# Performance work log

Measured on AMD Instinct MI355X. Metric: run time of the kernel, lower is better.

The kernel has to match this reference:

```python
import jax, jax.numpy as jnp
import numpy as np

U, I, H, E = 50000, 50000, 128, 800000


def segment_softmax(vals, seg, num):
    m = jax.ops.segment_max(vals, seg, num_segments=num)
    ex = jnp.exp(vals - m[seg])
    s = jax.ops.segment_sum(ex, seg, num_segments=num)
    return ex / s[seg]


def setup_inputs() -> dict:
    key = jax.random.key(0)
    ks = jax.random.split(key, 16)
    scale = 1.0 / np.sqrt(H)
    inp = {
        "u_emb": jax.random.normal(ks[0], (U, H), jnp.float32),
        "i_emb": jax.random.normal(ks[1], (I, H), jnp.float32),
        "pVui": jax.random.normal(ks[2], (E, H), jnp.float32),
        "pKiu": jax.random.normal(ks[3], (E, H), jnp.float32),
        "w1": jax.random.normal(ks[4], (H, H), jnp.float32) * scale,
        "w2": jax.random.normal(ks[5], (H, H), jnp.float32) * scale,
        "w1b": jax.random.normal(ks[6], (H, H), jnp.float32) * scale,
        "w2b": jax.random.normal(ks[7], (H, H), jnp.float32) * scale,
        "w3": jax.random.normal(ks[8], (H, H), jnp.float32) * scale,
        "w4": jax.random.normal(ks[9], (H, H), jnp.float32) * scale,
        "edge_index": jax.random.randint(ks[10], (2, E), 0, min(U, I), jnp.int64),
        "last_u": jax.random.randint(ks[11], (2, U), 0, I, jnp.int64),
        "last_i": jax.random.randint(ks[12], (2, I), 0, U, jnp.int64),
        "graph": jnp.zeros((1,), jnp.int64),
    }
    return inp


def reference(u_emb, i_emb, pVui, pKiu, w1, w2, w1b, w2b, w3, w4,
              edge_index, last_u, last_i, graph):
    sqrt_d = np.sqrt(float(u_emb.shape[1])).astype if False else float(np.sqrt(u_emb.shape[1]))
    nu, ni = u_emb.shape[0], i_emb.shape[0]
    src_u, dst_i = edge_index[0], edge_index[1]  # per-edge (user, item)

    # ---- longterm ----
    um_att = u_emb @ w2.T            # [U,H]
    im_att = i_emb @ w1.T            # [I,H]
    # sparse_dense_mul(edge_index, um_att @ im_att.T) -> per-edge dot products
    e_vals = jnp.sum(um_att[src_u] * im_att[dst_i], axis=-1)  # [E]
    e_ui = e_vals + jnp.sum(um_att[src_u] * pVui, axis=-1)
    alphas = segment_softmax(e_ui / sqrt_d, src_u, nu)        # softmax over items per user
    e_iu = e_vals + jnp.sum(im_att[dst_i] * pKiu, axis=-1)
    betas = segment_softmax(e_iu / sqrt_d, dst_i, ni)         # softmax over users per item
    um_b = u_emb @ w2b.T
    im_b = i_emb @ w1b.T
    hLu = jax.ops.segment_sum(alphas[:, None] * (im_b[dst_i] + pKiu), src_u, num_segments=nu)
    hLi = jax.ops.segment_sum(betas[:, None] * (um_b[src_u] + pVui), dst_i, num_segments=ni)

    # ---- shortterm ----
    last_item = i_emb[last_u[1]] @ w3.T   # [U,H] last item embedding per user
    last_user = u_emb[last_i[1]] @ w4.T   # [I,H] last user embedding per item
    a_vals = jnp.sum(last_item[src_u] * im_att[dst_i], axis=-1)
    s_alphas = segment_softmax(a_vals / sqrt_d, src_u, nu)
    b_vals = jnp.sum(last_user[src_u] * im_att[dst_i], axis=-1)
    s_betas = segment_softmax(b_vals / sqrt_d, dst_i, ni)
    # pass_messages with p = ones -> messages + 1
    hSu = jax.ops.segment_sum(s_alphas[:, None] * (im_att[dst_i] + 1.0), src_u, num_segments=nu)
    hSi = jax.ops.segment_sum(s_betas[:, None] * (um_att[src_u] + 1.0), dst_i, num_segments=ni)
    return (hLu, hSu, hLi, hSi)
```

## Files before the change

kernel.cpp:

```cpp
#include <hip/hip_runtime.h>
#include <hip/hip_bf16.h>
#include <math.h>


#define WB 1024

typedef float fvec4 __attribute__((ext_vector_type(4)));

__device__ __forceinline__ float4 nt_load4(const float* p) {
    fvec4 v = __builtin_nontemporal_load((const fvec4*)p);
    return make_float4(v.x, v.y, v.z, v.w);
}
__device__ __forceinline__ float dot4(float4 a, float4 b) {
    return a.x * b.x + a.y * b.y + a.z * b.z + a.w * b.w;
}
__device__ __forceinline__ void bfu(uint4 v, float4& lo, float4& hi) {
    lo.x = __uint_as_float(v.x << 16);
    lo.y = __uint_as_float(v.x & 0xFFFF0000u);
    lo.z = __uint_as_float(v.y << 16);
    lo.w = __uint_as_float(v.y & 0xFFFF0000u);
    hi.x = __uint_as_float(v.z << 16);
    hi.y = __uint_as_float(v.z & 0xFFFF0000u);
    hi.z = __uint_as_float(v.w << 16);
    hi.w = __uint_as_float(v.w & 0xFFFF0000u);
}
__device__ __forceinline__ unsigned rne16(float f) {
    unsigned u = __float_as_uint(f);
    return (u + 0x7FFFu + ((u >> 16) & 1u)) >> 16;
}
__device__ __forceinline__ unsigned pack2(float a, float b) {
    return rne16(a) | (rne16(b) << 16);
}

__global__ __launch_bounds__(256) void zero_kernel(int* __restrict__ p, int n)
{
    int i = blockIdx.x * 256 + threadIdx.x;
    if (i < n) p[i] = 0;
}

struct Gemm6Desc {
    const float* X[6];
    const float* W[6];
    unsigned short* O[6];
    const int*   g[6];
    int          ostride[6];
    int          nrows[6];
};

__global__ __launch_bounds__(256) void gemm6_kernel(Gemm6Desc d)
{
    __shared__ float Xl[64 * 32];
    __shared__ float Wl[128 * 32];
    const int j6 = blockIdx.y;
    const float* __restrict__ X = d.X[j6];
    const float* __restrict__ W = d.W[j6];
    unsigned short* __restrict__ O = d.O[j6];
    const int* __restrict__ gidx = d.g[j6];
    const int ostride = d.ostride[j6];
    const int nrows   = d.nrows[j6];

    const int t  = threadIdx.x;
    const int tx = t & 15;
    const int ty = t >> 4;
    const int brow = blockIdx.x * 64;
    if (brow >= nrows) return;

    float acc[4][8];
#pragma unroll
    for (int j = 0; j < 4; ++j)
#pragma unroll
        for (int i = 0; i < 8; ++i) acc[j][i] = 0.f;

    for (int k0 = 0; k0 < 128; k0 += 32) {
        __syncthreads();
#pragma unroll
        for (int u = 0; u < 2; ++u) {
            int idx4 = t + u * 256;
            int r  = idx4 >> 3;
            int k4 = idx4 & 7;
            int row = brow + r;
            float4 v = make_float4(0.f, 0.f, 0.f, 0.f);
            if (row < nrows) {
                int g = gidx ? gidx[row] : row;
                v = *(const float4*)(X + (size_t)g * 128 + k0 + k4 * 4);
            }
            int sw = k4 ^ ((r >> 3) & 7);
            *(float4*)(Xl + r * 32 + sw * 4) = v;
        }
#pragma unroll
        for (int u = 0; u < 4; ++u) {
            int idx4 = t + u * 256;
            int c  = idx4 >> 3;
            int k4 = idx4 & 7;
            float4 v = *(const float4*)(W + (size_t)c * 128 + k0 + k4 * 4);
            int sw = k4 ^ ((c >> 3) & 7);
            *(float4*)(Wl + c * 32 + sw * 4) = v;
        }
        __syncthreads();
#pragma unroll
        for (int k4 = 0; k4 < 8; ++k4) {
            float4 xv[4], wv[8];
#pragma unroll
            for (int j = 0; j < 4; ++j) {
                int r = ty * 4 + j;
                xv[j] = *(const float4*)(Xl + r * 32 + ((k4 ^ ((r >> 3) & 7)) * 4));
            }
#pragma unroll
            for (int i = 0; i < 8; ++i) {
                int c = tx * 8 + i;
                wv[i] = *(const float4*)(Wl + c * 32 + ((k4 ^ ((c >> 3) & 7)) * 4));
            }
#pragma unroll
            for (int j = 0; j < 4; ++j)
#pragma unroll
                for (int i = 0; i < 8; ++i) {
                    acc[j][i] += xv[j].x * wv[i].x;
                    acc[j][i] += xv[j].y * wv[i].y;
                    acc[j][i] += xv[j].z * wv[i].z;
                    acc[j][i] += xv[j].w * wv[i].w;
                }
        }
    }
    const int base = (tx < 8) ? (16 * tx) : (16 * (tx - 8) + 4);
#pragma unroll
    for (int j = 0; j < 4; ++j) {
        int row = brow + ty * 4 + j;
        if (row < nrows) {
            unsigned short* op = O + (size_t)row * ostride;
            uint2 lo, hi;
            lo.x = pack2(acc[j][0], acc[j][1]);
            lo.y = pack2(acc[j][2], acc[j][3]);
            hi.x = pack2(acc[j][4], acc[j][5]);
            hi.y = pack2(acc[j][6], acc[j][7]);
            *(uint2*)(op + base)     = lo;
            *(uint2*)(op + base + 8) = hi;
        }
    }
}

__global__ __launch_bounds__(256) void hist_kernel(
    const int* __restrict__ ei, int E,
    int* __restrict__ deg_u, int* __restrict__ deg_i)
{
    int e = blockIdx.x * 256 + threadIdx.x;
    if (e < E) {
        atomicAdd(&deg_u[ei[e]], 1);
        atomicAdd(&deg_i[ei[E + e]], 1);
    }
}

__global__ __launch_bounds__(256) void scan_blocksums_kernel(
    const int* __restrict__ deg_u, int nu, int nbu,
    const int* __restrict__ deg_i, int ni,
    int* __restrict__ bsum)
{
    int b = blockIdx.x;
    const int* deg; int n; int base;
    if (b < nbu) { deg = deg_u; n = nu; base = b * WB; }
    else         { deg = deg_i; n = ni; base = (b - nbu) * WB; }
    int t = threadIdx.x;
    int s = 0;
#pragma unroll
    for (int j = 0; j < 4; ++j) {
        int i = base + t * 4 + j;
        if (i < n) s += deg[i];
    }
#pragma unroll
    for (int o = 32; o > 0; o >>= 1) s += __shfl_xor(s, o);
    __shared__ int wt[4];
    if ((t & 63) == 0) wt[t >> 6] = s;
    __syncthreads();
    if (t == 0) bsum[b] = wt[0] + wt[1] + wt[2] + wt[3];
}

__global__ void scan_partials_kernel(
    const int* __restrict__ bsum, int* __restrict__ bscan,
    int nbu, int nbi,
    int* __restrict__ off_u, int nu, int* __restrict__ off_i, int ni)
{
    if (threadIdx.x != 0) return;
    if (blockIdx.x == 0) {
        int c = 0;
        for (int b = 0; b < nbu; ++b) { bscan[b] = c; c += bsum[b]; }
        off_u[nu] = c;
    } else {
        int c = 0;
        for (int b = 0; b < nbi; ++b) { bscan[nbu + b] = c; c += bsum[nbu + b]; }
        off_i[ni] = c;
    }
}

__global__ __launch_bounds__(256) void scan_final_kernel(
    const int* __restrict__ deg_u, int nu, int nbu,
    const int* __restrict__ deg_i, int ni,
    const int* __restrict__ bscan,
    int* __restrict__ off_u, int* __restrict__ cur_u,
    int* __restrict__ off_i, int* __restrict__ cur_i)
{
    int b = blockIdx.x;
    const int* deg; int n; int base; int* off; int* cur;
    if (b < nbu) { deg = deg_u; n = nu; base = b * WB; off = off_u; cur = cur_u; }
    else         { deg = deg_i; n = ni; base = (b - nbu) * WB; off = off_i; cur = cur_i; }
    int t = threadIdx.x;
    int lane = t & 63, w = t >> 6;
    int v[4];
    int s = 0;
#pragma unroll
    for (int j = 0; j < 4; ++j) {
        int i = base + t * 4 + j;
        v[j] = (i < n) ? deg[i] : 0;
        s += v[j];
    }
    int inc = s;
#pragma unroll
    for (int o = 1; o < 64; o <<= 1) {
        int x = __shfl_up(inc, o);
        if (lane >= o) inc += x;
    }
    int excl = inc - s;
    __shared__ int wt[4];
    if (lane == 63) wt[w] = inc;
    __syncthreads();
    int wbase = 0;
    for (int j = 0; j < w; ++j) wbase += wt[j];
    int e = bscan[b] + wbase + excl;
#pragma unroll
    for (int j = 0; j < 4; ++j) {
        int i = base + t * 4 + j;
        if (i < n) { off[i] = e; cur[i] = e; }
        e += v[j];
    }
}

__global__ __launch_bounds__(256) void scatter_ids_kernel(
    const int* __restrict__ ei, int E,
    int* __restrict__ cur_u, int* __restrict__ cur_i,
    int2* __restrict__ eu_list, int2* __restrict__ ei_list)
{
    int e = blockIdx.x * 256 + threadIdx.x;
    if (e < E) {
        int u = ei[e], v = ei[E + e];
        int pu = atomicAdd(&cur_u[u], 1);
        eu_list[pu] = make_int2(v, e);
        int pi = atomicAdd(&cur_i[v], 1);
        ei_list[pi] = make_int2(u, e);
    }
}

__global__ __launch_bounds__(256) void gather_u_kernel(
    const unsigned short* __restrict__ fusedU,
    const unsigned short* __restrict__ fusedI,
    const unsigned short* __restrict__ last_item,
    const unsigned short* __restrict__ last_user,
    const float* __restrict__ pVui, const float* __restrict__ pKiu,
    const int2* __restrict__ lst, const int* __restrict__ off_u,
    float2* __restrict__ x24,
    float* __restrict__ hLu, float* __restrict__ hSu, int U, float inv_sqrt_d)
{
    const int wv   = (int)(((size_t)blockIdx.x * blockDim.x + threadIdx.x) >> 6);
    const int lane = threadIdx.x & 63;
    const int g = lane >> 4;
    const int q = lane & 15;
    const int uid = wv * 4 + g;
    if (uid >= U) return;

    const uint4 umP = ((const uint4*)(fusedU    + (size_t)uid * 256))[q];
    const uint4 liP = ((const uint4*)(last_item + (size_t)uid * 128))[q];
    const uint4 luP = ((const uint4*)(last_user + (size_t)uid * 128))[q];

    float4 a1l = make_float4(0.f,0.f,0.f,0.f), a1h = make_float4(0.f,0.f,0.f,0.f);
    float4 a3l = make_float4(0.f,0.f,0.f,0.f), a3h = make_float4(0.f,0.f,0.f,0.f);
    float s1 = 0.f, s3 = 0.f;
    const int e0 = off_u[uid], e1 = off_u[uid + 1];

    int eA = e0, eB = e0 + 1;
    bool vA = eA < e1, vB = eB < e1;
    int2 rA = vA ? lst[eA] : make_int2(0, 0);
    int2 rB = vB ? lst[eB] : rA;

    while (vA) {
        int eA2 = eA + 2, eB2 = eB + 2;
        bool vA2 = eA2 < e1, vB2 = eB2 < e1;
        int2 rA2 = vA2 ? lst[eA2] : make_int2(0, 0);
        int2 rB2 = vB2 ? lst[eB2] : rA2;

        const uint4* fIA = (const uint4*)(fusedI + (size_t)rA.x * 256);
        const float* pvA = pVui + (size_t)rA.y * 128;
        const float* pkA = pKiu + (size_t)rA.y * 128;
        const uint4* fIB = (const uint4*)(fusedI + (size_t)rB.x * 256);
        const float* pvB = pVui + (size_t)rB.y * 128;
        const float* pkB = pKiu + (size_t)rB.y * 128;

        uint4 iaAp = fIA[q], ibAp = fIA[16 + q];
        uint4 iaBp = fIB[q], ibBp = fIB[16 + q];
        float4 pvA0 = nt_load4(pvA + q * 4), pvA1 = nt_load4(pvA + 64 + q * 4);
        float4 pkA0 = nt_load4(pkA + q * 4), pkA1 = nt_load4(pkA + 64 + q * 4);
        float4 pvB0 = nt_load4(pvB + q * 4), pvB1 = nt_load4(pvB + 64 + q * 4);
        float4 pkB0 = nt_load4(pkB + q * 4), pkB1 = nt_load4(pkB + 64 + q * 4);

        float4 iaA0, iaA1, iaB0, iaB1;
        bfu(iaAp, iaA0, iaA1);
        bfu(iaBp, iaB0, iaB1);

        float4 t0, t1;
        bfu(umP, t0, t1);
        float dA0 = dot4(t0, iaA0) + dot4(t1, iaA1);
        float qA1 = dA0 + dot4(t0, pvA0) + dot4(t1, pvA1);
        float dB0 = dot4(t0, iaB0) + dot4(t1, iaB1);
        float qB1 = dB0 + dot4(t0, pvB0) + dot4(t1, pvB1);
        float qA2 = dA0 + dot4(iaA0, pkA0) + dot4(iaA1, pkA1);
        float qB2 = dB0 + dot4(iaB0, pkB0) + dot4(iaB1, pkB1);
        bfu(liP, t0, t1);
        float qA3 = dot4(t0, iaA0) + dot4(t1, iaA1);
        float qB3 = dot4(t0, iaB0) + dot4(t1, iaB1);
        bfu(luP, t0, t1);
        float qA4 = dot4(t0, iaA0) + dot4(t1, iaA1);
        float qB4 = dot4(t0, iaB0) + dot4(t1, iaB1);
#pragma unroll
        for (int o = 8; o > 0; o >>= 1) {
            qA1 += __shfl_xor(qA1, o); qA2 += __shfl_xor(qA2, o);
            qA3 += __shfl_xor(qA3, o); qA4 += __shfl_xor(qA4, o);
            qB1 += __shfl_xor(qB1, o); qB2 += __shfl_xor(qB2, o);
            qB3 += __shfl_xor(qB3, o); qB4 += __shfl_xor(qB4, o);
        }
        float x1A = __expf(qA1 * inv_sqrt_d);
        float x2A = __expf(qA2 * inv_sqrt_d);
        float x3A = __expf(qA3 * inv_sqrt_d);
        float x4A = __expf(qA4 * inv_sqrt_d);
        float mB  = vB ? 1.f : 0.f;
        float x1B = __expf(qB1 * inv_sqrt_d) * mB;
        float x2B = __expf(qB2 * inv_sqrt_d);
        float x3B = __expf(qB3 * inv_sqrt_d) * mB;
        float x4B = __expf(qB4 * inv_sqrt_d);

        float4 ibA0, ibA1, ibB0, ibB1;
        bfu(ibAp, ibA0, ibA1);
        bfu(ibBp, ibB0, ibB1);
        a1l.x += x1A*(ibA0.x+pkA0.x) + x1B*(ibB0.x+pkB0.x);
        a1l.y += x1A*(ibA0.y+pkA0.y) + x1B*(ibB0.y+pkB0.y);
        a1l.z += x1A*(ibA0.z+pkA0.z) + x1B*(ibB0.z+pkB0.z);
        a1l.w += x1A*(ibA0.w+pkA0.w) + x1B*(ibB0.w+pkB0.w);
        a1h.x += x1A*(ibA1.x+pkA1.x) + x1B*(ibB1.x+pkB1.x);
        a1h.y += x1A*(ibA1.y+pkA1.y) + x1B*(ibB1.y+pkB1.y);
        a1h.z += x1A*(ibA1.z+pkA1.z) + x1B*(ibB1.z+pkB1.z);
        a1h.w += x1A*(ibA1.w+pkA1.w) + x1B*(ibB1.w+pkB1.w);
        a3l.x += x3A*(iaA0.x+1.f) + x3B*(iaB0.x+1.f);
        a3l.y += x3A*(iaA0.y+1.f) + x3B*(iaB0.y+1.f);
        a3l.z += x3A*(iaA0.z+1.f) + x3B*(iaB0.z+1.f);
        a3l.w += x3A*(iaA0.w+1.f) + x3B*(iaB0.w+1.f);
        a3h.x += x3A*(iaA1.x+1.f) + x3B*(iaB1.x+1.f);
        a3h.y += x3A*(iaA1.y+1.f) + x3B*(iaB1.y+1.f);
        a3h.z += x3A*(iaA1.z+1.f) + x3B*(iaB1.z+1.f);
        a3h.w += x3A*(iaA1.w+1.f) + x3B*(iaB1.w+1.f);
        s1 += x1A + x1B; s3 += x3A + x3B;
        if (q == 0) {
            x24[rA.y] = make_float2(x2A, x4A);
            if (vB) x24[rB.y] = make_float2(x2B, x4B);
        }
        eA = eA2; eB = eB2; vA = vA2; vB = vB2; rA = rA2; rB = rB2;
    }
    float r1 = (s1 > 0.f) ? 1.f / s1 : 0.f;
    float r3 = (s3 > 0.f) ? 1.f / s3 : 0.f;
    float4* oL = (float4*)(hLu + (size_t)uid * 128);
    float4* oS = (float4*)(hSu + (size_t)uid * 128);
    oL[q]      = make_float4(a1l.x*r1, a1l.y*r1, a1l.z*r1, a1l.w*r1);
    oL[q + 16] = make_float4(a1h.x*r1, a1h.y*r1, a1h.z*r1, a1h.w*r1);
    oS[q]      = make_float4(a3l.x*r3, a3l.y*r3, a3l.z*r3, a3l.w*r3);
    oS[q + 16] = make_float4(a3h.x*r3, a3h.y*r3, a3h.z*r3, a3h.w*r3);
}

__global__ __launch_bounds__(256) void gather_i_kernel(
    const unsigned short* __restrict__ fusedU,
    const float* __restrict__ pVui,
    const int2* __restrict__ lst, const int* __restrict__ off_i,
    const float2* __restrict__ x24,
    float* __restrict__ hLi, float* __restrict__ hSi, int I)
{
    const int wv   = (int)(((size_t)blockIdx.x * blockDim.x + threadIdx.x) >> 6);
    const int lane = threadIdx.x & 63;
    const int g = lane >> 4;
    const int q = lane & 15;
    const int iid = wv * 4 + g;
    if (iid >= I) return;

    float4 a2l = make_float4(0.f,0.f,0.f,0.f), a2h = make_float4(0.f,0.f,0.f,0.f);
    float4 a4l = make_float4(0.f,0.f,0.f,0.f), a4h = make_float4(0.f,0.f,0.f,0.f);
    float s2 = 0.f, s4 = 0.f;
    const int e0 = off_i[iid], e1 = off_i[iid + 1];

    int eA = e0, eB = e0 + 1;
    bool vA = eA < e1, vB = eB < e1;
    int2 rA = vA ? lst[eA] : make_int2(0, 0);
    int2 rB = vB ? lst[eB] : rA;
    float2 xA = vA ? x24[rA.y] : make_float2(0.f, 0.f);
    float2 xB = vB ? x24[rB.y] : make_float2(0.f, 0.f);

    while (vA) {
        int eA2 = eA + 2, eB2 = eB + 2;
        bool vA2 = eA2 < e1, vB2 = eB2 < e1;
        int2 rA2 = vA2 ? lst[eA2] : make_int2(0, 0);
        int2 rB2 = vB2 ? lst[eB2] : rA2;
        float2 xA2v = vA2 ? x24[rA2.y] : make_float2(0.f, 0.f);
        float2 xB2v = vB2 ? x24[rB2.y] : make_float2(0.f, 0.f);

        const uint4* fUA = (const uint4*)(fusedU + (size_t)rA.x * 256);
        const float* pvA = pVui + (size_t)rA.y * 128;
        const uint4* fUB = (const uint4*)(fusedU + (size_t)rB.x * 256);
        const float* pvB = pVui + (size_t)rB.y * 128;

        uint4 uaAp = fUA[q], ubAp = fUA[16 + q];
        uint4 uaBp = fUB[q], ubBp = fUB[16 + q];
        float4 pvA0 = nt_load4(pvA + q * 4), pvA1 = nt_load4(pvA + 64 + q * 4);
        float4 pvB0 = nt_load4(pvB + q * 4), pvB1 = nt_load4(pvB + 64 + q * 4);

        float4 uaA0, uaA1, ubA0, ubA1, uaB0, uaB1, ubB0, ubB1;
        bfu(uaAp, uaA0, uaA1); bfu(ubAp, ubA0, ubA1);
        bfu(uaBp, uaB0, uaB1); bfu(ubBp, ubB0, ubB1);

        if (!vB) { xB.x = 0.f; xB.y = 0.f; }
        a2l.x += xA.x*(ubA0.x+pvA0.x) + xB.x*(ubB0.x+pvB0.x);
        a2l.y += xA.x*(ubA0.y+pvA0.y) + xB.x*(ubB0.y+pvB0.y);
        a2l.z += xA.x*(ubA0.z+pvA0.z) + xB.x*(ubB0.z+pvB0.z);
        a2l.w += xA.x*(ubA0.w+pvA0.w) + xB.x*(ubB0.w+pvB0.w);
        a2h.x += xA.x*(ubA1.x+pvA1.x) + xB.x*(ubB1.x+pvB1.x);
        a2h.y += xA.x*(ubA1.y+pvA1.y) + xB.x*(ubB1.y+pvB1.y);
        a2h.z += xA.x*(ubA1.z+pvA1.z) + xB.x*(ubB1.z+pvB1.z);
        a2h.w += xA.x*(ubA1.w+pvA1.w) + xB.x*(ubB1.w+pvB1.w);
        a4l.x += xA.y*(uaA0.x+1.f) + xB.y*(uaB0.x+1.f);
        a4l.y += xA.y*(uaA0.y+1.f) + xB.y*(uaB0.y+1.f);
        a4l.z += xA.y*(uaA0.z+1.f) + xB.y*(uaB0.z+1.f);
        a4l.w += xA.y*(uaA0.w+1.f) + xB.y*(uaB0.w+1.f);
        a4h.x += xA.y*(uaA1.x+1.f) + xB.y*(uaB1.x+1.f);
        a4h.y += xA.y*(uaA1.y+1.f) + xB.y*(uaB1.y+1.f);
        a4h.z += xA.y*(uaA1.z+1.f) + xB.y*(uaB1.z+1.f);
        a4h.w += xA.y*(uaA1.w+1.f) + xB.y*(uaB1.w+1.f);
        s2 += xA.x + xB.x; s4 += xA.y + xB.y;

        eA = eA2; eB = eB2; vA = vA2; vB = vB2;
        rA = rA2; rB = rB2; xA = xA2v; xB = xB2v;
    }
    float r2 = (s2 > 0.f) ? 1.f / s2 : 0.f;
    float r4 = (s4 > 0.f) ? 1.f / s4 : 0.f;
    float4* oL = (float4*)(hLi + (size_t)iid * 128);
    float4* oS = (float4*)(hSi + (size_t)iid * 128);
    oL[q]      = make_float4(a2l.x*r2, a2l.y*r2, a2l.z*r2, a2l.w*r2);
    oL[q + 16] = make_float4(a2h.x*r2, a2h.y*r2, a2h.z*r2, a2h.w*r2);
    oS[q]      = make_float4(a4l.x*r4, a4l.y*r4, a4l.z*r4, a4l.w*r4);
    oS[q + 16] = make_float4(a4h.x*r4, a4h.y*r4, a4h.z*r4, a4h.w*r4);
}

extern "C" void kernel_launch(void* const* d_in, const int* in_sizes, int n_in,
                              void* d_out, int out_size, void* d_ws, size_t ws_size,
                              hipStream_t stream)
{
    const float* u_emb = (const float*)d_in[0];
    const float* i_emb = (const float*)d_in[1];
    const float* pVui  = (const float*)d_in[2];
    const float* pKiu  = (const float*)d_in[3];
    const float* w1    = (const float*)d_in[4];
    const float* w2    = (const float*)d_in[5];
    const float* w1b   = (const float*)d_in[6];
    const float* w2b   = (const float*)d_in[7];
    const float* w3    = (const float*)d_in[8];
    const float* w4    = (const float*)d_in[9];
    const int* edge_index = (const int*)d_in[10];
    const int* last_u     = (const int*)d_in[11];
    const int* last_i     = (const int*)d_in[12];

    const int U = in_sizes[0] / 128;
    const int I = in_sizes[1] / 128;
    const int E = in_sizes[10] / 2;
    const int nbu = (U + WB - 1) / WB;
    const int nbi = (I + WB - 1) / WB;

    unsigned short* us = (unsigned short*)d_ws;
    unsigned short* fusedU    = us;  us += (size_t)U * 256;
    unsigned short* fusedI    = us;  us += (size_t)I * 256;
    unsigned short* last_item = us;  us += (size_t)U * 128;
    unsigned short* last_user = us;  us += (size_t)I * 128;
    float* ws = (float*)us;
    float2* x24 = (float2*)ws;  ws += (size_t)E * 2;
    int2* eu_list = (int2*)ws;  ws += (size_t)E * 2;
    int2* ei_list = (int2*)ws;  ws += (size_t)E * 2;
    int* ip = (int*)ws;
    int* deg_u   = ip;  ip += U;
    int* deg_i   = ip;  ip += I;
    int* off_u   = ip;  ip += U + 1;
    int* off_i   = ip;  ip += I + 1;
    int* cur_u   = ip;  ip += U;
    int* cur_i   = ip;  ip += I;
    int* bsum    = ip;  ip += nbu + nbi;
    int* bscan   = ip;  ip += nbu + nbi;

    float* hLu = (float*)d_out;
    float* hSu = hLu + (size_t)U * 128;
    float* hLi = hSu + (size_t)U * 128;
    float* hSi = hLi + (size_t)I * 128;

    dim3 blk(256);
    const int eblk = (E + 255) / 256;
    zero_kernel<<<(U + I + 255) / 256, blk, 0, stream>>>(deg_u, U + I);
    hist_kernel<<<eblk, blk, 0, stream>>>(edge_index, E, deg_u, deg_i);
    scan_blocksums_kernel<<<nbu + nbi, blk, 0, stream>>>(deg_u, U, nbu, deg_i, I, bsum);
    scan_partials_kernel<<<2, 64, 0, stream>>>(bsum, bscan, nbu, nbi, off_u, U, off_i, I);
    scan_final_kernel<<<nbu + nbi, blk, 0, stream>>>(
        deg_u, U, nbu, deg_i, I, bscan, off_u, cur_u, off_i, cur_i);
    scatter_ids_kernel<<<eblk, blk, 0, stream>>>(
        edge_index, E, cur_u, cur_i, eu_list, ei_list);

    Gemm6Desc gd;
    gd.X[0] = u_emb; gd.W[0] = w2;  gd.O[0] = fusedU;       gd.g[0] = nullptr;    gd.ostride[0] = 256; gd.nrows[0] = U;
    gd.X[1] = u_emb; gd.W[1] = w2b; gd.O[1] = fusedU + 128; gd.g[1] = nullptr;    gd.ostride[1] = 256; gd.nrows[1] = U;
    gd.X[2] = i_emb; gd.W[2] = w1;  gd.O[2] = fusedI;       gd.g[2] = nullptr;    gd.ostride[2] = 256; gd.nrows[2] = I;
    gd.X[3] = i_emb; gd.W[3] = w1b; gd.O[3] = fusedI + 128; gd.g[3] = nullptr;    gd.ostride[3] = 256; gd.nrows[3] = I;
    gd.X[4] = i_emb; gd.W[4] = w3;  gd.O[4] = last_item;    gd.g[4] = last_u + U; gd.ostride[4] = 128; gd.nrows[4] = U;
    gd.X[5] = u_emb; gd.W[5] = w4;  gd.O[5] = last_user;    gd.g[5] = last_i + I; gd.ostride[5] = 128; gd.nrows[5] = I;
    int maxrows = (U > I) ? U : I;
    dim3 ggrid((maxrows + 63) / 64, 6);
    gemm6_kernel<<<ggrid, blk, 0, stream>>>(gd);

    const float inv_sqrt_d = 1.0f / sqrtf(128.0f);
    gather_u_kernel<<<(U + 15) / 16, blk, 0, stream>>>(
        fusedU, fusedI, last_item, last_user, pVui, pKiu, eu_list, off_u,
        x24, hLu, hSu, U, inv_sqrt_d);
    gather_i_kernel<<<(I + 15) / 16, blk, 0, stream>>>(
        fusedU, pVui, ei_list, off_i, x24, hLi, hSi, I);
}
```

Baseline: 709.3 us.

## Merge user and item gathers into one kernel, recomputing item scores

The separate user-side and item-side gather kernels are replaced by a single kernel whose blocks alternate between user segments and item segments, so both sides run concurrently in one launch. The x24 per-edge buffer of item softmax numerators is removed. The item side now recomputes its scores itself, gathering pKiu and last_user rows per edge. This drops the x24 write/read and the ordering dependency between the two kernels. In exchange, the item pass must stream all of pKiu a second time, adding a large amount of memory traffic.

New measurement: 871.2 us. 1.23x slower.

```diff
diff --git a/kernel.cpp b/kernel.cpp
--- a/kernel.cpp
+++ b/kernel.cpp
@@ -247,206 +247,213 @@
     }
 }
 
-__global__ __launch_bounds__(256) void gather_u_kernel(
+__global__ __launch_bounds__(256) void mega_gather_kernel(
     const unsigned short* __restrict__ fusedU,
     const unsigned short* __restrict__ fusedI,
     const unsigned short* __restrict__ last_item,
     const unsigned short* __restrict__ last_user,
     const float* __restrict__ pVui, const float* __restrict__ pKiu,
-    const int2* __restrict__ lst, const int* __restrict__ off_u,
-    float2* __restrict__ x24,
-    float* __restrict__ hLu, float* __restrict__ hSu, int U, float inv_sqrt_d)
-{
-    const int wv   = (int)(((size_t)blockIdx.x * blockDim.x + threadIdx.x) >> 6);
+    const int2* __restrict__ eu_list, const int* __restrict__ off_u,
+    const int2* __restrict__ ei_list, const int* __restrict__ off_i,
+    float* __restrict__ hLu, float* __restrict__ hSu,
+    float* __restrict__ hLi, float* __restrict__ hSi,
+    int U, int I, int nu_blk, int ni_blk, float inv_sqrt_d)
+{
+    const int bid = blockIdx.x;
+    int sel, blk;
+    const int mn = (nu_blk < ni_blk) ? nu_blk : ni_blk;
+    if (bid < 2 * mn) { sel = bid & 1; blk = bid >> 1; }
+    else {
+        int r = bid - 2 * mn;
+        if (nu_blk > ni_blk) { sel = 0; blk = mn + r; }
+        else                 { sel = 1; blk = mn + r; }
+    }
     const int lane = threadIdx.x & 63;
     const int g = lane >> 4;
     const int q = lane & 15;
-    const int uid = wv * 4 + g;
-    if (uid >= U) return;
-
-    const uint4 umP = ((const uint4*)(fusedU    + (size_t)uid * 256))[q];
-    const uint4 liP = ((const uint4*)(last_item + (size_t)uid * 128))[q];
-    const uint4 luP = ((const uint4*)(last_user + (size_t)uid * 128))[q];
-
-    float4 a1l = make_float4(0.f,0.f,0.f,0.f), a1h = make_float4(0.f,0.f,0.f,0.f);
-    float4 a3l = make_float4(0.f,0.f,0.f,0.f), a3h = make_float4(0.f,0.f,0.f,0.f);
-    float s1 = 0.f, s3 = 0.f;
-    const int e0 = off_u[uid], e1 = off_u[uid + 1];
-
-    int eA = e0, eB = e0 + 1;
-    bool vA = eA < e1, vB = eB < e1;
-    int2 rA = vA ? lst[eA] : make_int2(0, 0);
-    int2 rB = vB ? lst[eB] : rA;
-
-    while (vA) {
-        int eA2 = eA + 2, eB2 = eB + 2;
-        bool vA2 = eA2 < e1, vB2 = eB2 < e1;
-        int2 rA2 = vA2 ? lst[eA2] : make_int2(0, 0);
-        int2 rB2 = vB2 ? lst[eB2] : rA2;
-
-        const uint4* fIA = (const uint4*)(fusedI + (size_t)rA.x * 256);
-        const float* pvA = pVui + (size_t)rA.y * 128;
-        const float* pkA = pKiu + (size_t)rA.y * 128;
-        const uint4* fIB = (const uint4*)(fusedI + (size_t)rB.x * 256);
-        const float* pvB = pVui + (size_t)rB.y * 128;
-        const float* pkB = pKiu + (size_t)rB.y * 128;
-
-        uint4 iaAp = fIA[q], ibAp = fIA[16 + q];
-        uint4 iaBp = fIB[q], ibBp = fIB[16 + q];
-        float4 pvA0 = nt_load4(pvA + q * 4), pvA1 = nt_load4(pvA + 64 + q * 4);
-        float4 pkA0 = nt_load4(pkA + q * 4), pkA1 = nt_load4(pkA + 64 + q * 4);
-        float4 pvB0 = nt_load4(pvB + q * 4), pvB1 = nt_load4(pvB + 64 + q * 4);
-        float4 pkB0 = nt_load4(pkB + q * 4), pkB1 = nt_load4(pkB + 64 + q * 4);
-
-        float4 iaA0, iaA1, iaB0, iaB1;
-        bfu(iaAp, iaA0, iaA1);
-        bfu(iaBp, iaB0, iaB1);
-
-        float4 t0, t1;
-        bfu(umP, t0, t1);
-        float dA0 = dot4(t0, iaA0) + dot4(t1, iaA1);
-        float qA1 = dA0 + dot4(t0, pvA0) + dot4(t1, pvA1);
-        float dB0 = dot4(t0, iaB0) + dot4(t1, iaB1);
-        float qB1 = dB0 + dot4(t0, pvB0) + dot4(t1, pvB1);
-        float qA2 = dA0 + dot4(iaA0, pkA0) + dot4(iaA1, pkA1);
-        float qB2 = dB0 + dot4(iaB0, pkB0) + dot4(iaB1, pkB1);
-        bfu(liP, t0, t1);
-        float qA3 = dot4(t0, iaA0) + dot4(t1, iaA1);
-        float qB3 = dot4(t0, iaB0) + dot4(t1, iaB1);
-        bfu(luP, t0, t1);
-        float qA4 = dot4(t0, iaA0) + dot4(t1, iaA1);
-        float qB4 = dot4(t0, iaB0) + dot4(t1, iaB1);
-#pragma unroll
-        for (int o = 8; o > 0; o >>= 1) {
-            qA1 += __shfl_xor(qA1, o); qA2 += __shfl_xor(qA2, o);
-            qA3 += __shfl_xor(qA3, o); qA4 += __shfl_xor(qA4, o);
-            qB1 += __shfl_xor(qB1, o); qB2 += __shfl_xor(qB2, o);
-            qB3 += __shfl_xor(qB3, o); qB4 += __shfl_xor(qB4, o);
+    const int seg = blk * 16 + (threadIdx.x >> 6) * 4 + g;
+
+    if (sel == 0) {
+        const int uid = seg;
+        if (uid >= U) return;
+        const uint4 umP = ((const uint4*)(fusedU    + (size_t)uid * 256))[q];
+        const uint4 liP = ((const uint4*)(last_item + (size_t)uid * 128))[q];
+
+        float4 a1l = make_float4(0.f,0.f,0.f,0.f), a1h = make_float4(0.f,0.f,0.f,0.f);
+        float4 a3l = make_float4(0.f,0.f,0.f,0.f), a3h = make_float4(0.f,0.f,0.f,0.f);
+        float s1 = 0.f, s3 = 0.f;
+        const int e0 = off_u[uid], e1 = off_u[uid + 1];
+
+        int eA = e0, eB = e0 + 1;
+        bool vA = eA < e1, vB = eB < e1;
+        int2 rA = vA ? eu_list[eA] : make_int2(0, 0);
+        int2 rB = vB ? eu_list[eB] : rA;
+
+        while (vA) {
+            int eA2 = eA + 2, eB2 = eB + 2;
+            bool vA2 = eA2 < e1, vB2 = eB2 < e1;
+            int2 rA2 = vA2 ? eu_list[eA2] : make_int2(0, 0);
+            int2 rB2 = vB2 ? eu_list[eB2] : rA2;
+
+            const uint4* fIA = (const uint4*)(fusedI + (size_t)rA.x * 256);
+            const float* pvA = pVui + (size_t)rA.y * 128;
+            const float* pkA = pKiu + (size_t)rA.y * 128;
+            const uint4* fIB = (const uint4*)(fusedI + (size_t)rB.x * 256);
+            const float* pvB = pVui + (size_t)rB.y * 128;
+            const float* pkB = pKiu + (size_t)rB.y * 128;
+
+            uint4 iaAp = fIA[q], ibAp = fIA[16 + q];
+            uint4 iaBp = fIB[q], ibBp = fIB[16 + q];
+            float4 pvA0 = nt_load4(pvA + q * 4), pvA1 = nt_load4(pvA + 64 + q * 4);
+            float4 pkA0 = nt_load4(pkA + q * 4), pkA1 = nt_load4(pkA + 64 + q * 4);
+            float4 pvB0 = nt_load4(pvB + q * 4), pvB1 = nt_load4(pvB + 64 + q * 4);
+            float4 pkB0 = nt_load4(pkB + q * 4), pkB1 = nt_load4(pkB + 64 + q * 4);
+
+            float4 iaA0, iaA1, iaB0, iaB1, t0, t1;
+            bfu(iaAp, iaA0, iaA1);
+            bfu(iaBp, iaB0, iaB1);
+            bfu(umP, t0, t1);
+            float qA1 = dot4(t0, iaA0) + dot4(t1, iaA1)
+                      + dot4(t0, pvA0) + dot4(t1, pvA1);
+            float qB1 = dot4(t0, iaB0) + dot4(t1, iaB1)
+                      + dot4(t0, pvB0) + dot4(t1, pvB1);
+            bfu(liP, t0, t1);
+            float qA3 = dot4(t0, iaA0) + dot4(t1, iaA1);
+            float qB3 = dot4(t0, iaB0) + dot4(t1, iaB1);
+#pragma unroll
+            for (int o = 8; o > 0; o >>= 1) {
+                qA1 += __shfl_xor(qA1, o); qA3 += __shfl_xor(qA3, o);
+                qB1 += __shfl_xor(qB1, o); qB3 += __shfl_xor(qB3, o);
+            }
+            float x1A = __expf(qA1 * inv_sqrt_d);
+            float x3A = __expf(qA3 * inv_sqrt_d);
+            float mB  = vB ? 1.f : 0.f;
+            float x1B = __expf(qB1 * inv_sqrt_d) * mB;
+            float x3B = __expf(qB3 * inv_sqrt_d) * mB;
+
+            float4 ibA0, ibA1, ibB0, ibB1;
+            bfu(ibAp, ibA0, ibA1);
+            bfu(ibBp, ibB0, ibB1);
+            a1l.x += x1A*(ibA0.x+pkA0.x) + x1B*(ibB0.x+pkB0.x);
+            a1l.y += x1A*(ibA0.y+pkA0.y) + x1B*(ibB0.y+pkB0.y);
+            a1l.z += x1A*(ibA0.z+pkA0.z) + x1B*(ibB0.z+pkB0.z);
+            a1l.w += x1A*(ibA0.w+pkA0.w) + x1B*(ibB0.w+pkB0.w);
+            a1h.x += x1A*(ibA1.x+pkA1.x) + x1B*(ibB1.x+pkB1.x);
+            a1h.y += x1A*(ibA1.y+pkA1.y) + x1B*(ibB1.y+pkB1.y);
+            a1h.z += x1A*(ibA1.z+pkA1.z) + x1B*(ibB1.z+pkB1.z);
+            a1h.w += x1A*(ibA1.w+pkA1.w) + x1B*(ibB1.w+pkB1.w);
+            a3l.x += x3A*(iaA0.x+1.f) + x3B*(iaB0.x+1.f);
+            a3l.y += x3A*(iaA0.y+1.f) + x3B*(iaB0.y+1.f);
+            a3l.z += x3A*(iaA0.z+1.f) + x3B*(iaB0.z+1.f);
+            a3l.w += x3A*(iaA0.w+1.f) + x3B*(iaB0.w+1.f);
+            a3h.x += x3A*(iaA1.x+1.f) + x3B*(iaB1.x+1.f);
+            a3h.y += x3A*(iaA1.y+1.f) + x3B*(iaB1.y+1.f);
+            a3h.z += x3A*(iaA1.z+1.f) + x3B*(iaB1.z+1.f);
+            a3h.w += x3A*(iaA1.w+1.f) + x3B*(iaB1.w+1.f);
+            s1 += x1A + x1B; s3 += x3A + x3B;
+
+            eA = eA2; eB = eB2; vA = vA2; vB = vB2; rA = rA2; rB = rB2;
         }
-        float x1A = __expf(qA1 * inv_sqrt_d);
-        float x2A = __expf(qA2 * inv_sqrt_d);
-        float x3A = __expf(qA3 * inv_sqrt_d);
-        float x4A = __expf(qA4 * inv_sqrt_d);
-        float mB  = vB ? 1.f : 0.f;
-        float x1B = __expf(qB1 * inv_sqrt_d) * mB;
-        float x2B = __expf(qB2 * inv_sqrt_d);
-        float x3B = __expf(qB3 * inv_sqrt_d) * mB;
-        float x4B = __expf(qB4 * inv_sqrt_d);
-
-        float4 ibA0, ibA1, ibB0, ibB1;
-        bfu(ibAp, ibA0, ibA1);
-        bfu(ibBp, ibB0, ibB1);
-        a1l.x += x1A*(ibA0.x+pkA0.x) + x1B*(ibB0.x+pkB0.x);
-        a1l.y += x1A*(ibA0.y+pkA0.y) + x1B*(ibB0.y+pkB0.y);
-        a1l.z += x1A*(ibA0.z+pkA0.z) + x1B*(ibB0.z+pkB0.z);
-        a1l.w += x1A*(ibA0.w+pkA0.w) + x1B*(ibB0.w+pkB0.w);
-        a1h.x += x1A*(ibA1.x+pkA1.x) + x1B*(ibB1.x+pkB1.x);
-        a1h.y += x1A*(ibA1.y+pkA1.y) + x1B*(ibB1.y+pkB1.y);
-        a1h.z += x1A*(ibA1.z+pkA1.z) + x1B*(ibB1.z+pkB1.z);
-        a1h.w += x1A*(ibA1.w+pkA1.w) + x1B*(ibB1.w+pkB1.w);
-        a3l.x += x3A*(iaA0.x+1.f) + x3B*(iaB0.x+1.f);
-        a3l.y += x3A*(iaA0.y+1.f) + x3B*(iaB0.y+1.f);
-        a3l.z += x3A*(iaA0.z+1.f) + x3B*(iaB0.z+1.f);
-        a3l.w += x3A*(iaA0.w+1.f) + x3B*(iaB0.w+1.f);
-        a3h.x += x3A*(iaA1.x+1.f) + x3B*(iaB1.x+1.f);
-        a3h.y += x3A*(iaA1.y+1.f) + x3B*(iaB1.y+1.f);
-        a3h.z += x3A*(iaA1.z+1.f) + x3B*(iaB1.z+1.f);
-        a3h.w += x3A*(iaA1.w+1.f) + x3B*(iaB1.w+1.f);
-        s1 += x1A + x1B; s3 += x3A + x3B;
-        if (q == 0) {
-            x24[rA.y] = make_float2(x2A, x4A);
-            if (vB) x24[rB.y] = make_float2(x2B, x4B);
+        float r1 = (s1 > 0.f) ? 1.f / s1 : 0.f;
+        float r3 = (s3 > 0.f) ? 1.f / s3 : 0.f;
+        float4* oL = (float4*)(hLu + (size_t)uid * 128);
+        float4* oS = (float4*)(hSu + (size_t)uid * 128);
+        oL[q]      = make_float4(a1l.x*r1, a1l.y*r1, a1l.z*r1, a1l.w*r1);
+        oL[q + 16] = make_float4(a1h.x*r1, a1h.y*r1, a1h.z*r1, a1h.w*r1);
+        oS[q]      = make_float4(a3l.x*r3, a3l.y*r3, a3l.z*r3, a3l.w*r3);
+        oS[q + 16] = make_float4(a3h.x*r3, a3h.y*r3, a3h.z*r3, a3h.w*r3);
+    } else {
+        const int iid = seg;
+        if (iid >= I) return;
+        const uint4 imP = ((const uint4*)(fusedI + (size_t)iid * 256))[q];
+
+        float4 a2l = make_float4(0.f,0.f,0.f,0.f), a2h = make_float4(0.f,0.f,0.f,0.f);
+        float4 a4l = make_float4(0.f,0.f,0.f,0.f), a4h = make_float4(0.f,0.f,0.f,0.f);
+        float s2 = 0.f, s4 = 0.f;
+        const int e0 = off_i[iid], e1 = off_i[iid + 1];
+
+        int eA = e0, eB = e0 + 1;
+        bool vA = eA < e1, vB = eB < e1;
+        int2 rA = vA ? ei_list[eA] : make_int2(0, 0);
+        int2 rB = vB ? ei_list[eB] : rA;
+
+        while (vA) {
+            int eA2 = eA + 2, eB2 = eB + 2;
+            bool vA2 = eA2 < e1, vB2 = eB2 < e1;
+            int2 rA2 = vA2 ? ei_list[eA2] : make_int2(0, 0);
+            int2 rB2 = vB2 ? ei_list[eB2] : rA2;
+
+            const uint4* fUA = (const uint4*)(fusedU + (size_t)rA.x * 256);
+            const float* pvA = pVui + (size_t)rA.y * 128;
+            const float* pkA = pKiu + (size_t)rA.y * 128;
+            const uint4 luAp = ((const uint4*)(last_user + (size_t)rA.x * 128))[q];
+            const uint4* fUB = (const uint4*)(fusedU + (size_t)rB.x * 256);
+            const float* pvB = pVui + (size_t)rB.y * 128;
+            const float* pkB = pKiu + (size_t)rB.y * 128;
+            const uint4 luBp = ((const uint4*)(last_user + (size_t)rB.x * 128))[q];
+
+            uint4 uaAp = fUA[q], ubAp = fUA[16 + q];
+            uint4 uaBp = fUB[q], ubBp = fUB[16 + q];
+            float4 pvA0 = nt_load4(pvA + q * 4), pvA1 = nt_load4(pvA + 64 + q * 4);
+            float4 pkA0 = nt_load4(pkA + q * 4), pkA1 = nt_load4(pkA + 64 + q * 4);
+            float4 pvB0 = nt_load4(pvB + q * 4), pvB1 = nt_load4(pvB + 64 + q * 4);
+            float4 pkB0 = nt_load4(pkB + q * 4), pkB1 = nt_load4(pkB + 64 + q * 4);
+
+            float4 m0, m1, uaA0, uaA1, uaB0, uaB1, t0, t1;
+            bfu(imP, m0, m1);
+            bfu(uaAp, uaA0, uaA1);
+            bfu(uaBp, uaB0, uaB1);
+            float qA2 = dot4(uaA0, m0) + dot4(uaA1, m1)
+                      + dot4(m0, pkA0) + dot4(m1, pkA1);
+            float qB2 = dot4(uaB0, m0) + dot4(uaB1, m1)
+                      + dot4(m0, pkB0) + dot4(m1, pkB1);
+            bfu(luAp, t0, t1);
+            float qA4 = dot4(t0, m0) + dot4(t1, m1);
+            bfu(luBp, t0, t1);
+            float qB4 = dot4(t0, m0) + dot4(t1, m1);
+#pragma unroll
+            for (int o = 8; o > 0; o >>= 1) {
+                qA2 += __shfl_xor(qA2, o); qA4 += __shfl_xor(qA4, o);
+                qB2 += __shfl_xor(qB2, o); qB4 += __shfl_xor(qB4, o);
+            }
+            float x2A = __expf(qA2 * inv_sqrt_d);
+            float x4A = __expf(qA4 * inv_sqrt_d);
+            float mB  = vB ? 1.f : 0.f;
+            float x2B = __expf(qB2 * inv_sqrt_d) * mB;
+            float x4B = __expf(qB4 * inv_sqrt_d) * mB;
+
+            float4 ubA0, ubA1, ubB0, ubB1;
+            bfu(ubAp, ubA0, ubA1);
+            bfu(ubBp, ubB0, ubB1);
+            a2l.x += x2A*(ubA0.x+pvA0.x) + x2B*(ubB0.x+pvB0.x);
+            a2l.y += x2A*(ubA0.y+pvA0.y) + x2B*(ubB0.y+pvB0.y);
+            a2l.z += x2A*(ubA0.z+pvA0.z) + x2B*(ubB0.z+pvB0.z);
+            a2l.w += x2A*(ubA0.w+pvA0.w) + x2B*(ubB0.w+pvB0.w);
+            a2h.x += x2A*(ubA1.x+pvA1.x) + x2B*(ubB1.x+pvB1.x);
+            a2h.y += x2A*(ubA1.y+pvA1.y) + x2B*(ubB1.y+pvB1.y);
+            a2h.z += x2A*(ubA1.z+pvA1.z) + x2B*(ubB1.z+pvB1.z);
+            a2h.w += x2A*(ubA1.w+pvA1.w) + x2B*(ubB1.w+pvB1.w);
+            a4l.x += x4A*(uaA0.x+1.f) + x4B*(uaB0.x+1.f);
+            a4l.y += x4A*(uaA0.y+1.f) + x4B*(uaB0.y+1.f);
+            a4l.z += x4A*(uaA0.z+1.f) + x4B*(uaB0.z+1.f);
+            a4l.w += x4A*(uaA0.w+1.f) + x4B*(uaB0.w+1.f);
+            a4h.x += x4A*(uaA1.x+1.f) + x4B*(uaB1.x+1.f);
+            a4h.y += x4A*(uaA1.y+1.f) + x4B*(uaB1.y+1.f);
+            a4h.z += x4A*(uaA1.z+1.f) + x4B*(uaB1.z+1.f);
+            a4h.w += x4A*(uaA1.w+1.f) + x4B*(uaB1.w+1.f);
+            s2 += x2A + x2B; s4 += x4A + x4B;
+
+            eA = eA2; eB = eB2; vA = vA2; vB = vB2; rA = rA2; rB = rB2;
         }
-        eA = eA2; eB = eB2; vA = vA2; vB = vB2; rA = rA2; rB = rB2;
-    }
-    float r1 = (s1 > 0.f) ? 1.f / s1 : 0.f;
-    float r3 = (s3 > 0.f) ? 1.f / s3 : 0.f;
-    float4* oL = (float4*)(hLu + (size_t)uid * 128);
-    float4* oS = (float4*)(hSu + (size_t)uid * 128);
-    oL[q]      = make_float4(a1l.x*r1, a1l.y*r1, a1l.z*r1, a1l.w*r1);
-    oL[q + 16] = make_float4(a1h.x*r1, a1h.y*r1, a1h.z*r1, a1h.w*r1);
-    oS[q]      = make_float4(a3l.x*r3, a3l.y*r3, a3l.z*r3, a3l.w*r3);
-    oS[q + 16] = make_float4(a3h.x*r3, a3h.y*r3, a3h.z*r3, a3h.w*r3);
-}
-
-__global__ __launch_bounds__(256) void gather_i_kernel(
-    const unsigned short* __restrict__ fusedU,
-    const float* __restrict__ pVui,
-    const int2* __restrict__ lst, const int* __restrict__ off_i,
-    const float2* __restrict__ x24,
-    float* __restrict__ hLi, float* __restrict__ hSi, int I)
-{
-    const int wv   = (int)(((size_t)blockIdx.x * blockDim.x + threadIdx.x) >> 6);
-    const int lane = threadIdx.x & 63;
-    const int g = lane >> 4;
-    const int q = lane & 15;
-    const int iid = wv * 4 + g;
-    if (iid >= I) return;
-
-    float4 a2l = make_float4(0.f,0.f,0.f,0.f), a2h = make_float4(0.f,0.f,0.f,0.f);
-    float4 a4l = make_float4(0.f,0.f,0.f,0.f), a4h = make_float4(0.f,0.f,0.f,0.f);
-    float s2 = 0.f, s4 = 0.f;
-    const int e0 = off_i[iid], e1 = off_i[iid + 1];
-
-    int eA = e0, eB = e0 + 1;
-    bool vA = eA < e1, vB = eB < e1;
-    int2 rA = vA ? lst[eA] : make_int2(0, 0);
-    int2 rB = vB ? lst[eB] : rA;
-    float2 xA = vA ? x24[rA.y] : make_float2(0.f, 0.f);
-    float2 xB = vB ? x24[rB.y] : make_float2(0.f, 0.f);
-
-    while (vA) {
-        int eA2 = eA + 2, eB2 = eB + 2;
-        bool vA2 = eA2 < e1, vB2 = eB2 < e1;
-        int2 rA2 = vA2 ? lst[eA2] : make_int2(0, 0);
-        int2 rB2 = vB2 ? lst[eB2] : rA2;
-        float2 xA2v = vA2 ? x24[rA2.y] : make_float2(0.f, 0.f);
-        float2 xB2v = vB2 ? x24[rB2.y] : make_float2(0.f, 0.f);
-
-        const uint4* fUA = (const uint4*)(fusedU + (size_t)rA.x * 256);
-        const float* pvA = pVui + (size_t)rA.y * 128;
-        const uint4* fUB = (const uint4*)(fusedU + (size_t)rB.x * 256);
-        const float* pvB = pVui + (size_t)rB.y * 128;
-
-        uint4 uaAp = fUA[q], ubAp = fUA[16 + q];
-        uint4 uaBp = fUB[q], ubBp = fUB[16 + q];
-        float4 pvA0 = nt_load4(pvA + q * 4), pvA1 = nt_load4(pvA + 64 + q * 4);
-        float4 pvB0 = nt_load4(pvB + q * 4), pvB1 = nt_load4(pvB + 64 + q * 4);
-
-        float4 uaA0, uaA1, ubA0, ubA1, uaB0, uaB1, ubB0, ubB1;
-        bfu(uaAp, uaA0, uaA1); bfu(ubAp, ubA0, ubA1);
-        bfu(uaBp, uaB0, uaB1); bfu(ubBp, ubB0, ubB1);
-
-        if (!vB) { xB.x = 0.f; xB.y = 0.f; }
-        a2l.x += xA.x*(ubA0.x+pvA0.x) + xB.x*(ubB0.x+pvB0.x);
-        a2l.y += xA.x*(ubA0.y+pvA0.y) + xB.x*(ubB0.y+pvB0.y);
-        a2l.z += xA.x*(ubA0.z+pvA0.z) + xB.x*(ubB0.z+pvB0.z);
-        a2l.w += xA.x*(ubA0.w+pvA0.w) + xB.x*(ubB0.w+pvB0.w);
-        a2h.x += xA.x*(ubA1.x+pvA1.x) + xB.x*(ubB1.x+pvB1.x);
-        a2h.y += xA.x*(ubA1.y+pvA1.y) + xB.x*(ubB1.y+pvB1.y);
-        a2h.z += xA.x*(ubA1.z+pvA1.z) + xB.x*(ubB1.z+pvB1.z);
-        a2h.w += xA.x*(ubA1.w+pvA1.w) + xB.x*(ubB1.w+pvB1.w);
-        a4l.x += xA.y*(uaA0.x+1.f) + xB.y*(uaB0.x+1.f);
-        a4l.y += xA.y*(uaA0.y+1.f) + xB.y*(uaB0.y+1.f);
-        a4l.z += xA.y*(uaA0.z+1.f) + xB.y*(uaB0.z+1.f);
-        a4l.w += xA.y*(uaA0.w+1.f) + xB.y*(uaB0.w+1.f);
-        a4h.x += xA.y*(uaA1.x+1.f) + xB.y*(uaB1.x+1.f);
-        a4h.y += xA.y*(uaA1.y+1.f) + xB.y*(uaB1.y+1.f);
-        a4h.z += xA.y*(uaA1.z+1.f) + xB.y*(uaB1.z+1.f);
-        a4h.w += xA.y*(uaA1.w+1.f) + xB.y*(uaB1.w+1.f);
-        s2 += xA.x + xB.x; s4 += xA.y + xB.y;
-
-        eA = eA2; eB = eB2; vA = vA2; vB = vB2;
-        rA = rA2; rB = rB2; xA = xA2v; xB = xB2v;
-    }
-    float r2 = (s2 > 0.f) ? 1.f / s2 : 0.f;
-    float r4 = (s4 > 0.f) ? 1.f / s4 : 0.f;
-    float4* oL = (float4*)(hLi + (size_t)iid * 128);
-    float4* oS = (float4*)(hSi + (size_t)iid * 128);
-    oL[q]      = make_float4(a2l.x*r2, a2l.y*r2, a2l.z*r2, a2l.w*r2);
-    oL[q + 16] = make_float4(a2h.x*r2, a2h.y*r2, a2h.z*r2, a2h.w*r2);
-    oS[q]      = make_float4(a4l.x*r4, a4l.y*r4, a4l.z*r4, a4l.w*r4);
-    oS[q + 16] = make_float4(a4h.x*r4, a4h.y*r4, a4h.z*r4, a4h.w*r4);
+        float r2 = (s2 > 0.f) ? 1.f / s2 : 0.f;
+        float r4 = (s4 > 0.f) ? 1.f / s4 : 0.f;
+        float4* oL = (float4*)(hLi + (size_t)iid * 128);
+        float4* oS = (float4*)(hSi + (size_t)iid * 128);
+        oL[q]      = make_float4(a2l.x*r2, a2l.y*r2, a2l.z*r2, a2l.w*r2);
+        oL[q + 16] = make_float4(a2h.x*r2, a2h.y*r2, a2h.z*r2, a2h.w*r2);
+        oS[q]      = make_float4(a4l.x*r4, a4l.y*r4, a4l.z*r4, a4l.w*r4);
+        oS[q + 16] = make_float4(a4h.x*r4, a4h.y*r4, a4h.z*r4, a4h.w*r4);
+    }
 }
 
 extern "C" void kernel_launch(void* const* d_in, const int* in_sizes, int n_in,
@@ -479,7 +486,6 @@
     unsigned short* last_item = us;  us += (size_t)U * 128;
     unsigned short* last_user = us;  us += (size_t)I * 128;
     float* ws = (float*)us;
-    float2* x24 = (float2*)ws;  ws += (size_t)E * 2;
     int2* eu_list = (int2*)ws;  ws += (size_t)E * 2;
     int2* ei_list = (int2*)ws;  ws += (size_t)E * 2;
     int* ip = (int*)ws;
@@ -520,9 +526,10 @@
     gemm6_kernel<<<ggrid, blk, 0, stream>>>(gd);
 
     const float inv_sqrt_d = 1.0f / sqrtf(128.0f);
-    gather_u_kernel<<<(U + 15) / 16, blk, 0, stream>>>(
-        fusedU, fusedI, last_item, last_user, pVui, pKiu, eu_list, off_u,
-        x24, hLu, hSu, U, inv_sqrt_d);
-    gather_i_kernel<<<(I + 15) / 16, blk, 0, stream>>>(
-        fusedU, pVui, ei_list, off_i, x24, hLi, hSi, I);
-}
+    const int nu_blk = (U + 15) / 16;
+    const int ni_blk = (I + 15) / 16;
+    mega_gather_kernel<<<nu_blk + ni_blk, blk, 0, stream>>>(
+        fusedU, fusedI, last_item, last_user, pVui, pKiu,
+        eu_list, off_u, ei_list, off_i,
+        hLu, hSu, hLi, hSi, U, I, nu_blk, ni_blk, inv_sqrt_d);
+}
```
